# Kernel tuning notes

Hardware: AMD Instinct MI355X
Metric: run time of the kernel (lower is better)

Reference implementation:

```python
import jax, jax.numpy as jnp
import numpy as np

N = 100000
E = 3200000
F_IN, H1, H2, C = 128, 64, 32, 10


def setup_inputs() -> dict:
    key = jax.random.key(0)
    ks = jax.random.split(key, 8)
    x = jax.random.normal(ks[0], (N, F_IN), dtype=jnp.float32)
    edge_index = jax.random.randint(ks[1], (2, E), 0, N, dtype=jnp.int64)
    W1 = jax.random.normal(ks[2], (F_IN, H1), dtype=jnp.float32) / np.sqrt(F_IN)
    b1 = jnp.zeros((H1,), dtype=jnp.float32)
    W2 = jax.random.normal(ks[3], (H1, H2), dtype=jnp.float32) / np.sqrt(H1)
    b2 = jnp.zeros((H2,), dtype=jnp.float32)
    Wc = jax.random.normal(ks[4], (H2, C), dtype=jnp.float32) / np.sqrt(H2)
    bc = jnp.zeros((C,), dtype=jnp.float32)
    return {"x": x, "edge_index": edge_index, "W1": W1, "b1": b1,
            "W2": W2, "b2": b2, "Wc": Wc, "bc": bc}


def gcn_conv(x, src, dst, W, b, n):
    # PyG GCNConv: x' = D^{-1/2} (A + I) D^{-1/2} (X W) + b
    h = x @ W                                        # [N, H]
    ones = jnp.ones((src.shape[0],), dtype=h.dtype)
    deg = jax.ops.segment_sum(ones, dst, num_segments=n) + 1.0  # +1 self loop
    dinv = jax.lax.rsqrt(deg)                        # deg >= 1, safe
    norm = dinv[src] * dinv[dst]                     # [E]
    msg = h[src] * norm[:, None]                     # [E, H] gather + scale
    agg = jax.ops.segment_sum(msg, dst, num_segments=n)
    # self-loop contribution: norm_ii = 1/deg_i
    out = agg + h * (dinv * dinv)[:, None]
    return out + b


def reference(x, edge_index, W1, b1, W2, b2, Wc, bc):
    n = x.shape[0]
    src, dst = edge_index[0], edge_index[1]
    h = gcn_conv(x, src, dst, W1, b1, n)
    h = jax.nn.relu(h)
    # dropout is identity in eval mode (training=False)
    h = gcn_conv(h, src, dst, W2, b2, n)
    h = jax.nn.relu(h)
    logits = h @ Wc + bc
    return jax.nn.log_softmax(logits, axis=1)
```

## Files before the change

kernel.cpp:

```cpp
#include <hip/hip_runtime.h>


#define BSHIFT 8
#define BMASK 255
#define NBUCK_MAX 512
#define TILE 4096
#define EPT 16
#define NPW 4
#define SCAP 12288

__device__ __forceinline__ unsigned pack_bf16(float lo, float hi) {
    unsigned ul = __float_as_uint(lo);
    ul = (ul + 0x7FFFu + ((ul >> 16) & 1u)) >> 16;
    unsigned uh = __float_as_uint(hi);
    uh = ((uh + 0x7FFFu + ((uh >> 16) & 1u)) >> 16) << 16;
    return ul | uh;
}

__global__ void k_hist(const int* __restrict__ dst, int* __restrict__ bcnt, int E) {
    __shared__ int h[NBUCK_MAX];
    for (int i = threadIdx.x; i < NBUCK_MAX; i += blockDim.x) h[i] = 0;
    __syncthreads();
    for (int e = blockIdx.x * blockDim.x + threadIdx.x; e < E; e += gridDim.x * blockDim.x)
        atomicAdd(&h[dst[e] >> BSHIFT], 1);
    __syncthreads();
    for (int i = threadIdx.x; i < NBUCK_MAX; i += blockDim.x)
        if (h[i]) atomicAdd(&bcnt[i], h[i]);
}

__global__ __launch_bounds__(256) void k_binA(const int* __restrict__ src,
                                              const int* __restrict__ dst,
                                              const int* __restrict__ bcnt,
                                              int* __restrict__ gcur0,
                                              int* __restrict__ binned, int E) {
    __shared__ int hist[NBUCK_MAX];
    __shared__ int lbase[NBUCK_MAX];
    __shared__ int gbase[NBUCK_MAX];
    __shared__ int gdelta[NBUCK_MAX];
    __shared__ int cnt2[NBUCK_MAX];
    __shared__ int scanb[256];
    __shared__ int scanc[256];
    __shared__ int stage[TILE];
    __shared__ unsigned short sbucket[TILE];

    int t = threadIdx.x;
    for (int i = t; i < NBUCK_MAX; i += 256) { hist[i] = 0; cnt2[i] = 0; }
    int c0 = bcnt[2 * t], c1 = bcnt[2 * t + 1];
    int cs = c0 + c1;
    scanc[t] = cs;
    __syncthreads();
    for (int o = 1; o < 256; o <<= 1) {
        int u = (t >= o) ? scanc[t - o] : 0;
        __syncthreads();
        scanc[t] += u;
        __syncthreads();
    }
    int ex2 = scanc[t] - cs;
    gbase[2 * t] = ex2;
    gbase[2 * t + 1] = ex2 + c0;
    __syncthreads();

    int tileStart = blockIdx.x * TILE;
    int cntTile = min(TILE, E - tileStart);

    int vals[EPT];
    int bks[EPT];
#pragma unroll
    for (int i = 0; i < EPT; i++) {
        int e = tileStart + t + i * 256;
        if (e < E) {
            int s = src[e], d = dst[e];
            vals[i] = s | ((d & BMASK) << 17);
            bks[i] = d >> BSHIFT;
            atomicAdd(&hist[bks[i]], 1);
        } else bks[i] = -1;
    }
    __syncthreads();

    int a0 = hist[2 * t], a1 = hist[2 * t + 1];
    int ts = a0 + a1;
    scanb[t] = ts;
    __syncthreads();
    for (int o = 1; o < 256; o <<= 1) {
        int u = (t >= o) ? scanb[t - o] : 0;
        __syncthreads();
        scanb[t] += u;
        __syncthreads();
    }
    int ex = scanb[t] - ts;
    lbase[2 * t] = ex;
    lbase[2 * t + 1] = ex + a0;
    __syncthreads();

    for (int b = t; b < NBUCK_MAX; b += 256) {
        int c = hist[b];
        int g = c ? (gbase[b] + atomicAdd(&gcur0[b], c)) : 0;
        gdelta[b] = g - lbase[b];
    }
#pragma unroll
    for (int i = 0; i < EPT; i++) {
        if (bks[i] >= 0) {
            int rr = atomicAdd(&cnt2[bks[i]], 1);
            int slot = lbase[bks[i]] + rr;
            stage[slot] = vals[i];
            sbucket[slot] = (unsigned short)bks[i];
        }
    }
    __syncthreads();
    for (int i = t; i < cntTile; i += 256) {
        int b = sbucket[i];
        binned[gdelta[b] + i] = stage[i];
    }
}

__global__ __launch_bounds__(256) void k_sortcsr(const int* __restrict__ bcnt,
                                                 const int* __restrict__ binned,
                                                 int* __restrict__ rowptr,
                                                 float* __restrict__ dinv,
                                                 int* __restrict__ csr, int n, int E) {
    __shared__ int cnt[256];
    __shared__ int sc[256];
    __shared__ int rpl[256];
    __shared__ int lcur[256];
    __shared__ int gbase[NBUCK_MAX];
    __shared__ int scanc[256];
    __shared__ int stage2[SCAP];
    int b = blockIdx.x, t = threadIdx.x;
    cnt[t] = 0; lcur[t] = 0;
    int c0 = bcnt[2 * t], c1 = bcnt[2 * t + 1];
    int cs = c0 + c1;
    scanc[t] = cs;
    __syncthreads();
    for (int o = 1; o < 256; o <<= 1) {
        int u = (t >= o) ? scanc[t - o] : 0;
        __syncthreads();
        scanc[t] += u;
        __syncthreads();
    }
    int ex2 = scanc[t] - cs;
    gbase[2 * t] = ex2;
    gbase[2 * t + 1] = ex2 + c0;
    __syncthreads();

    int beg = gbase[b];
    int end = (b + 1 < NBUCK_MAX) ? gbase[b + 1] : E;
    for (int i = beg + t; i < end; i += 256)
        atomicAdd(&cnt[(binned[i] >> 17) & BMASK], 1);
    __syncthreads();
    int v = cnt[t];
    sc[t] = v;
    __syncthreads();
    for (int o = 1; o < 256; o <<= 1) {
        int u = (t >= o) ? sc[t - o] : 0;
        __syncthreads();
        sc[t] += u;
        __syncthreads();
    }
    int rp = beg + sc[t] - v;
    rpl[t] = rp;
    int g = (b << BSHIFT) + t;
    if (g < n) {
        rowptr[g] = rp;
        dinv[g] = rsqrtf((float)v + 1.0f);
        if (g == n - 1) rowptr[n] = E;
    }
    __syncthreads();
    for (int i = beg + t; i < end; i += 256) {
        int vv = binned[i];
        int ln = (vv >> 17) & BMASK;
        int k = atomicAdd(&lcur[ln], 1);
        int idx = rpl[ln] + k - beg;
        if (idx < SCAP) stage2[idx] = vv & 0x1FFFF;
        else            csr[beg + idx] = vv & 0x1FFFF;
    }
    __syncthreads();
    int cc = end - beg;
    for (int i = t; i < cc; i += 256)
        if (i < SCAP) csr[beg + i] = stage2[i];
}

template<int K, int M, int R>
__global__ __launch_bounds__(256) void k_gemm(const float* __restrict__ X,
                                              const float* __restrict__ W,
                                              const float* __restrict__ dinv,
                                              unsigned* __restrict__ hsb, int n) {
    constexpr int MW = M / 4;
    __shared__ float Ws[K * M];
    for (int i = threadIdx.x; i < K * M; i += 256) Ws[i] = W[i];
    __syncthreads();
    int w = threadIdx.x >> 6, lane = threadIdx.x & 63;
    int wo = w * MW;
    int r0 = blockIdx.x * (64 * R) + lane;
    float acc[R][MW];
#pragma unroll
    for (int i = 0; i < R; i++)
#pragma unroll
        for (int j = 0; j < MW; j++) acc[i][j] = 0.f;

    for (int k = 0; k < K; k += 4) {
        float4 xv[R];
#pragma unroll
        for (int i = 0; i < R; i++) {
            int rr = r0 + 64 * i;
            xv[i] = (rr < n) ? *(const float4*)(X + (size_t)rr * K + k)
                             : make_float4(0.f, 0.f, 0.f, 0.f);
        }
#pragma unroll
        for (int kk = 0; kk < 4; kk++) {
#pragma unroll
            for (int j = 0; j < MW; j += 4) {
                float4 wv = *(const float4*)&Ws[(k + kk) * M + wo + j];
#pragma unroll
                for (int i = 0; i < R; i++) {
                    float xs = (kk == 0) ? xv[i].x : (kk == 1) ? xv[i].y
                             : (kk == 2) ? xv[i].z : xv[i].w;
                    acc[i][j + 0] += xs * wv.x;
                    acc[i][j + 1] += xs * wv.y;
                    acc[i][j + 2] += xs * wv.z;
                    acc[i][j + 3] += xs * wv.w;
                }
            }
        }
    }
#pragma unroll
    for (int i = 0; i < R; i++) {
        int rr = r0 + 64 * i;
        if (rr < n) {
            float di = dinv[rr];
            unsigned p[MW / 2];
#pragma unroll
            for (int jj = 0; jj < MW / 2; jj++)
                p[jj] = pack_bf16(acc[i][2 * jj] * di, acc[i][2 * jj + 1] * di);
            unsigned* hr = hsb + (size_t)rr * (M / 2) + wo / 2;
#pragma unroll
            for (int jj = 0; jj < MW / 2; jj += 4)
                *(uint4*)(hr + jj) = make_uint4(p[jj], p[jj + 1], p[jj + 2], p[jj + 3]);
        }
    }
}

#define ACC8(V) \
    acc[0] += __uint_as_float((V).x << 16);  acc[1] += __uint_as_float((V).x & 0xFFFF0000u); \
    acc[2] += __uint_as_float((V).y << 16);  acc[3] += __uint_as_float((V).y & 0xFFFF0000u); \
    acc[4] += __uint_as_float((V).z << 16);  acc[5] += __uint_as_float((V).z & 0xFFFF0000u); \
    acc[6] += __uint_as_float((V).w << 16);  acc[7] += __uint_as_float((V).w & 0xFFFF0000u);

__global__ __launch_bounds__(256) void k_agg64f(
        const int* __restrict__ rowptr, const int* __restrict__ csr,
        const uint4* __restrict__ hsb, const float* __restrict__ dinv,
        const float* __restrict__ b1, const float* __restrict__ W2,
        unsigned* __restrict__ hsb2, int n) {
    int wid = (blockIdx.x * blockDim.x + threadIdx.x) >> 6;
    int lane = threadIdx.x & 63;
    int q = lane >> 3, r = lane & 7;
    int d0 = wid * NPW;
    if (d0 >= n) return;
    float w2r[8][4];
    float b1r[8];
#pragma unroll
    for (int i = 0; i < 8; i++) {
        b1r[i] = b1[8 * r + i];
#pragma unroll
        for (int jj = 0; jj < 4; jj++)
            w2r[i][jj] = W2[(8 * r + i) * 32 + 4 * q + jj];
    }
    int dend = min(d0 + NPW, n);
    int rp = rowptr[min(d0 + min(lane, NPW), n)];
    int beg = __shfl(rp, 0, 64);
    int end = __shfl(rp, 1, 64);
    int cc = min(end - beg, 64);
    int idxv = (lane < cc) ? csr[beg + lane] : 0;
    for (int d = d0; d < dend; d++) {
        int kk = d - d0;
        int nbeg = __shfl(rp, min(kk + 1, NPW), 64);
        int nend = __shfl(rp, min(kk + 2, NPW), 64);
        int ncc = min(nend - nbeg, 64);
        int nidxv = 0;
        if (d + 1 < dend) nidxv = (lane < ncc) ? csr[nbeg + lane] : 0;
        uint4 wsf = hsb[(size_t)d * 8 + r];
        float di = dinv[d];
        float acc[8];
#pragma unroll
        for (int i = 0; i < 8; i++) acc[i] = 0.f;
        int j = 0;
        for (; j + 16 <= cc; j += 16) {
            int sA = __shfl(idxv, j + q, 64);
            int sB = __shfl(idxv, j + 8 + q, 64);
            uint4 wA = hsb[(size_t)sA * 8 + r];
            uint4 wB = hsb[(size_t)sB * 8 + r];
            ACC8(wA)
            ACC8(wB)
        }
        {
            int tA = j + q, tB = j + 8 + q;
            int sA = __shfl(idxv, tA & 63, 64);
            int sB = __shfl(idxv, tB & 63, 64);
            if (tA < cc) { uint4 wv = hsb[(size_t)sA * 8 + r]; ACC8(wv) }
            if (tB < cc) { uint4 wv = hsb[(size_t)sB * 8 + r]; ACC8(wv) }
        }
        for (int c = beg + 64; c < end; c += 16) {
            if (c + q < end)     { uint4 wv = hsb[(size_t)csr[c + q] * 8 + r]; ACC8(wv) }
            if (c + 8 + q < end) { uint4 wv = hsb[(size_t)csr[c + 8 + q] * 8 + r]; ACC8(wv) }
        }
#pragma unroll
        for (int i = 0; i < 8; i++) {
            acc[i] += __shfl_xor(acc[i], 8, 64);
            acc[i] += __shfl_xor(acc[i], 16, 64);
            acc[i] += __shfl_xor(acc[i], 32, 64);
        }
        ACC8(wsf)
        float v[8];
#pragma unroll
        for (int i = 0; i < 8; i++) v[i] = fmaxf(acc[i] * di + b1r[i], 0.f);
        float h[4] = {0.f, 0.f, 0.f, 0.f};
#pragma unroll
        for (int i = 0; i < 8; i++)
#pragma unroll
            for (int jj = 0; jj < 4; jj++) h[jj] += v[i] * w2r[i][jj];
#pragma unroll
        for (int jj = 0; jj < 4; jj++) {
            h[jj] += __shfl_xor(h[jj], 1, 64);
            h[jj] += __shfl_xor(h[jj], 2, 64);
            h[jj] += __shfl_xor(h[jj], 4, 64);
        }
        if (r == 0) {
            unsigned p0 = pack_bf16(h[0] * di, h[1] * di);
            unsigned p1 = pack_bf16(h[2] * di, h[3] * di);
            *(uint2*)(hsb2 + (size_t)d * 16 + 2 * q) = make_uint2(p0, p1);
        }
        beg = nbeg; end = nend; cc = ncc; idxv = nidxv;
    }
}

__global__ __launch_bounds__(256) void k_agg32f(
        const int* __restrict__ rowptr, const int* __restrict__ csr,
        const uint4* __restrict__ hsb2, const float* __restrict__ dinv,
        const float* __restrict__ b2, const float* __restrict__ Wc,
        const float* __restrict__ bc, float* __restrict__ out, int n) {
    int wid = (blockIdx.x * blockDim.x + threadIdx.x) >> 6;
    int lane = threadIdx.x & 63;
    int q = lane >> 2, r = lane & 3;
    int d0 = wid * NPW;
    if (d0 >= n) return;
    float wcr[8];
    float b2r[8];
    float bcr = (q < 10) ? bc[q] : 0.f;
#pragma unroll
    for (int i = 0; i < 8; i++) {
        b2r[i] = b2[8 * r + i];
        wcr[i] = (q < 10) ? Wc[(8 * r + i) * 10 + q] : 0.f;
    }
    int dend = min(d0 + NPW, n);
    int rp = rowptr[min(d0 + min(lane, NPW), n)];
    int beg = __shfl(rp, 0, 64);
    int end = __shfl(rp, 1, 64);
    int cc = min(end - beg, 64);
    int idxv = (lane < cc) ? csr[beg + lane] : 0;
    for (int d = d0; d < dend; d++) {
        int kk = d - d0;
        int nbeg = __shfl(rp, min(kk + 1, NPW), 64);
        int nend = __shfl(rp, min(kk + 2, NPW), 64);
        int ncc = min(nend - nbeg, 64);
        int nidxv = 0;
        if (d + 1 < dend) nidxv = (lane < ncc) ? csr[nbeg + lane] : 0;
        uint4 wsf = hsb2[(size_t)d * 4 + r];
        float di = dinv[d];
        float acc[8];
#pragma unroll
        for (int i = 0; i < 8; i++) acc[i] = 0.f;
        int j = 0;
        for (; j + 32 <= cc; j += 32) {
            int sA = __shfl(idxv, j + q, 64);
            int sB = __shfl(idxv, j + 16 + q, 64);
            uint4 wA = hsb2[(size_t)sA * 4 + r];
            uint4 wB = hsb2[(size_t)sB * 4 + r];
            ACC8(wA)
            ACC8(wB)
        }
        {
            int tA = j + q, tB = j + 16 + q;
            int sA = __shfl(idxv, tA & 63, 64);
            int sB = __shfl(idxv, tB & 63, 64);
            if (tA < cc) { uint4 wv = hsb2[(size_t)sA * 4 + r]; ACC8(wv) }
            if (tB < cc) { uint4 wv = hsb2[(size_t)sB * 4 + r]; ACC8(wv) }
        }
        for (int c = beg + 64; c < end; c += 32) {
            if (c + q < end)      { uint4 wv = hsb2[(size_t)csr[c + q] * 4 + r]; ACC8(wv) }
            if (c + 16 + q < end) { uint4 wv = hsb2[(size_t)csr[c + 16 + q] * 4 + r]; ACC8(wv) }
        }
#pragma unroll
        for (int i = 0; i < 8; i++) {
            acc[i] += __shfl_xor(acc[i], 4, 64);
            acc[i] += __shfl_xor(acc[i], 8, 64);
            acc[i] += __shfl_xor(acc[i], 16, 64);
            acc[i] += __shfl_xor(acc[i], 32, 64);
        }
        ACC8(wsf)
        float part = 0.f;
#pragma unroll
        for (int i = 0; i < 8; i++) {
            float v = fmaxf(acc[i] * di + b2r[i], 0.f);
            part += v * wcr[i];
        }
        part += __shfl_xor(part, 1, 64);
        part += __shfl_xor(part, 2, 64);
        float mylogit = part + bcr;
        float m = -1e30f;
        float l[10];
#pragma unroll
        for (int c = 0; c < 10; c++) {
            l[c] = __shfl(mylogit, 4 * c, 64);
            m = fmaxf(m, l[c]);
        }
        float ssum = 0.f;
#pragma unroll
        for (int c = 0; c < 10; c++) ssum += __expf(l[c] - m);
        float lse = m + __logf(ssum);
        if (r == 0 && q < 10) out[(size_t)d * 10 + q] = mylogit - lse;
        beg = nbeg; end = nend; cc = ncc; idxv = nidxv;
    }
}

extern "C" void kernel_launch(void* const* d_in, const int* in_sizes, int n_in,
                              void* d_out, int out_size, void* d_ws, size_t ws_size,
                              hipStream_t stream) {
    const float* x  = (const float*)d_in[0];
    const int*   ei = (const int*)d_in[1];
    const float* W1 = (const float*)d_in[2];
    const float* b1 = (const float*)d_in[3];
    const float* W2 = (const float*)d_in[4];
    const float* b2 = (const float*)d_in[5];
    const float* Wc = (const float*)d_in[6];
    const float* bc = (const float*)d_in[7];
    float* out = (float*)d_out;

    const int N = in_sizes[0] / 128;
    const int E = in_sizes[1] / 2;
    const int* src = ei;
    const int* dst = ei + E;

    const int NBUCK = (N + BMASK) >> BSHIFT;
    const int NTILE = (E + TILE - 1) / TILE;
    const int NW = (N + NPW - 1) / NPW;

    char* ws = (char*)d_ws;
    size_t off = 0;
    auto alloc = [&](size_t elems) {
        void* p = ws + off;
        off += ((elems * 4 + 1023) & ~(size_t)1023);
        return p;
    };
    float*    dinv   = (float*)alloc(N);
    int*      bcnt   = (int*)alloc(NBUCK_MAX);
    int*      gcur0  = (int*)alloc(NBUCK_MAX);
    int*      rowptr = (int*)alloc(N + 1);
    int*      binned = (int*)alloc(E);
    int*      csr    = (int*)alloc(E);
    unsigned* hsb    = (unsigned*)alloc((size_t)N * 32);
    unsigned* hsb2   = (unsigned*)alloc((size_t)N * 16);

    hipMemsetAsync(bcnt, 0, sizeof(int) * NBUCK_MAX * 2, stream);

    k_hist<<<512, 256, 0, stream>>>(dst, bcnt, E);
    k_binA<<<NTILE, 256, 0, stream>>>(src, dst, bcnt, gcur0, binned, E);
    k_sortcsr<<<NBUCK, 256, 0, stream>>>(bcnt, binned, rowptr, dinv, csr, N, E);

    k_gemm<128, 64, 2><<<(N + 127) / 128, 256, 0, stream>>>(x, W1, dinv, hsb, N);
    k_agg64f<<<(NW * 64 + 255) / 256, 256, 0, stream>>>(rowptr, csr, (const uint4*)hsb,
                                                        dinv, b1, W2, hsb2, N);
    k_agg32f<<<(NW * 64 + 255) / 256, 256, 0, stream>>>(rowptr, csr, (const uint4*)hsb2,
                                                        dinv, b2, Wc, bc, out, N);
}
```

Baseline: 359.6 us.

## Split layer-1 aggregation into feature-sliced gather passes plus separate finalize kernel

```diff
diff --git a/kernel.cpp b/kernel.cpp
--- a/kernel.cpp
+++ b/kernel.cpp
@@ -183,7 +183,7 @@
 __global__ __launch_bounds__(256) void k_gemm(const float* __restrict__ X,
                                               const float* __restrict__ W,
                                               const float* __restrict__ dinv,
-                                              unsigned* __restrict__ hsb, int n) {
+                                              unsigned* __restrict__ hsbS, int n) {
     constexpr int MW = M / 4;
     __shared__ float Ws[K * M];
     for (int i = threadIdx.x; i < K * M; i += 256) Ws[i] = W[i];
@@ -231,23 +231,71 @@
 #pragma unroll
             for (int jj = 0; jj < MW / 2; jj++)
                 p[jj] = pack_bf16(acc[i][2 * jj] * di, acc[i][2 * jj + 1] * di);
-            unsigned* hr = hsb + (size_t)rr * (M / 2) + wo / 2;
-#pragma unroll
-            for (int jj = 0; jj < MW / 2; jj += 4)
-                *(uint4*)(hr + jj) = make_uint4(p[jj], p[jj + 1], p[jj + 2], p[jj + 3]);
-        }
-    }
-}
-
-#define ACC8(V) \
-    acc[0] += __uint_as_float((V).x << 16);  acc[1] += __uint_as_float((V).x & 0xFFFF0000u); \
-    acc[2] += __uint_as_float((V).y << 16);  acc[3] += __uint_as_float((V).y & 0xFFFF0000u); \
-    acc[4] += __uint_as_float((V).z << 16);  acc[5] += __uint_as_float((V).z & 0xFFFF0000u); \
-    acc[6] += __uint_as_float((V).w << 16);  acc[7] += __uint_as_float((V).w & 0xFFFF0000u);
-
-__global__ __launch_bounds__(256) void k_agg64f(
+            unsigned* hr = hsbS + ((size_t)w * n + rr) * 8;
+            *(uint4*)(hr + 0) = make_uint4(p[0], p[1], p[2], p[3]);
+            *(uint4*)(hr + 4) = make_uint4(p[4], p[5], p[6], p[7]);
+        }
+    }
+}
+
+__global__ __launch_bounds__(256) void k_aggp(
         const int* __restrict__ rowptr, const int* __restrict__ csr,
-        const uint4* __restrict__ hsb, const float* __restrict__ dinv,
+        const unsigned* __restrict__ hsbS, float* __restrict__ agg, int n) {
+    int b = blockIdx.x;
+    int s = b & 3;
+    int ib = b >> 2;
+    int wid = ib * 4 + (threadIdx.x >> 6);
+    int lane = threadIdx.x & 63;
+    int e = lane >> 3, f = lane & 7;
+    int d0 = wid * NPW;
+    if (d0 >= n) return;
+    const unsigned* tab = hsbS + (size_t)s * n * 8;
+    int dend = min(d0 + NPW, n);
+    int rp = rowptr[min(d0 + min(lane, NPW), n)];
+    int beg = __shfl(rp, 0, 64);
+    int end = __shfl(rp, 1, 64);
+    int cc = min(end - beg, 64);
+    int idxv = (lane < cc) ? __builtin_nontemporal_load(&csr[beg + lane]) : 0;
+    for (int d = d0; d < dend; d++) {
+        int kk = d - d0;
+        int nbeg = __shfl(rp, min(kk + 1, NPW), 64);
+        int nend = __shfl(rp, min(kk + 2, NPW), 64);
+        int ncc = min(nend - nbeg, 64);
+        int nidxv = 0;
+        if (d + 1 < dend) nidxv = (lane < ncc) ? __builtin_nontemporal_load(&csr[nbeg + lane]) : 0;
+        unsigned wsf = tab[(size_t)d * 8 + f];
+        float a0 = 0.f, a1 = 0.f;
+#pragma unroll
+        for (int g = 0; g < 8; g++) {
+            int slot = 8 * g + e;
+            int sg = __shfl(idxv, slot, 64);
+            if (slot < cc) {
+                unsigned wv = tab[(size_t)sg * 8 + f];
+                a0 += __uint_as_float(wv << 16);
+                a1 += __uint_as_float(wv & 0xFFFF0000u);
+            }
+        }
+        for (int c = beg + 64; c < end; c += 8) {
+            if (c + e < end) {
+                int sx = __builtin_nontemporal_load(&csr[c + e]);
+                unsigned wv = tab[(size_t)sx * 8 + f];
+                a0 += __uint_as_float(wv << 16);
+                a1 += __uint_as_float(wv & 0xFFFF0000u);
+            }
+        }
+        a0 += __shfl_xor(a0, 8, 64);  a1 += __shfl_xor(a1, 8, 64);
+        a0 += __shfl_xor(a0, 16, 64); a1 += __shfl_xor(a1, 16, 64);
+        a0 += __shfl_xor(a0, 32, 64); a1 += __shfl_xor(a1, 32, 64);
+        a0 += __uint_as_float(wsf << 16);
+        a1 += __uint_as_float(wsf & 0xFFFF0000u);
+        if (e == 0)
+            *(float2*)(agg + ((size_t)d * 4 + s) * 16 + 2 * f) = make_float2(a0, a1);
+        beg = nbeg; end = nend; cc = ncc; idxv = nidxv;
+    }
+}
+
+__global__ __launch_bounds__(256) void k_fin64(
+        const float* __restrict__ agg, const float* __restrict__ dinv,
         const float* __restrict__ b1, const float* __restrict__ W2,
         unsigned* __restrict__ hsb2, int n) {
     int wid = (blockIdx.x * blockDim.x + threadIdx.x) >> 6;
@@ -265,53 +313,19 @@
             w2r[i][jj] = W2[(8 * r + i) * 32 + 4 * q + jj];
     }
     int dend = min(d0 + NPW, n);
-    int rp = rowptr[min(d0 + min(lane, NPW), n)];
-    int beg = __shfl(rp, 0, 64);
-    int end = __shfl(rp, 1, 64);
-    int cc = min(end - beg, 64);
-    int idxv = (lane < cc) ? csr[beg + lane] : 0;
     for (int d = d0; d < dend; d++) {
-        int kk = d - d0;
-        int nbeg = __shfl(rp, min(kk + 1, NPW), 64);
-        int nend = __shfl(rp, min(kk + 2, NPW), 64);
-        int ncc = min(nend - nbeg, 64);
-        int nidxv = 0;
-        if (d + 1 < dend) nidxv = (lane < ncc) ? csr[nbeg + lane] : 0;
-        uint4 wsf = hsb[(size_t)d * 8 + r];
+        float4 x0 = *(const float4*)(agg + (size_t)d * 64 + 8 * r);
+        float4 x1 = *(const float4*)(agg + (size_t)d * 64 + 8 * r + 4);
         float di = dinv[d];
-        float acc[8];
-#pragma unroll
-        for (int i = 0; i < 8; i++) acc[i] = 0.f;
-        int j = 0;
-        for (; j + 16 <= cc; j += 16) {
-            int sA = __shfl(idxv, j + q, 64);
-            int sB = __shfl(idxv, j + 8 + q, 64);
-            uint4 wA = hsb[(size_t)sA * 8 + r];
-            uint4 wB = hsb[(size_t)sB * 8 + r];
-            ACC8(wA)
-            ACC8(wB)
-        }
-        {
-            int tA = j + q, tB = j + 8 + q;
-            int sA = __shfl(idxv, tA & 63, 64);
-            int sB = __shfl(idxv, tB & 63, 64);
-            if (tA < cc) { uint4 wv = hsb[(size_t)sA * 8 + r]; ACC8(wv) }
-            if (tB < cc) { uint4 wv = hsb[(size_t)sB * 8 + r]; ACC8(wv) }
-        }
-        for (int c = beg + 64; c < end; c += 16) {
-            if (c + q < end)     { uint4 wv = hsb[(size_t)csr[c + q] * 8 + r]; ACC8(wv) }
-            if (c + 8 + q < end) { uint4 wv = hsb[(size_t)csr[c + 8 + q] * 8 + r]; ACC8(wv) }
-        }
-#pragma unroll
-        for (int i = 0; i < 8; i++) {
-            acc[i] += __shfl_xor(acc[i], 8, 64);
-            acc[i] += __shfl_xor(acc[i], 16, 64);
-            acc[i] += __shfl_xor(acc[i], 32, 64);
-        }
-        ACC8(wsf)
         float v[8];
-#pragma unroll
-        for (int i = 0; i < 8; i++) v[i] = fmaxf(acc[i] * di + b1r[i], 0.f);
+        v[0] = fmaxf(x0.x * di + b1r[0], 0.f);
+        v[1] = fmaxf(x0.y * di + b1r[1], 0.f);
+        v[2] = fmaxf(x0.z * di + b1r[2], 0.f);
+        v[3] = fmaxf(x0.w * di + b1r[3], 0.f);
+        v[4] = fmaxf(x1.x * di + b1r[4], 0.f);
+        v[5] = fmaxf(x1.y * di + b1r[5], 0.f);
+        v[6] = fmaxf(x1.z * di + b1r[6], 0.f);
+        v[7] = fmaxf(x1.w * di + b1r[7], 0.f);
         float h[4] = {0.f, 0.f, 0.f, 0.f};
 #pragma unroll
         for (int i = 0; i < 8; i++)
@@ -328,9 +342,14 @@
             unsigned p1 = pack_bf16(h[2] * di, h[3] * di);
             *(uint2*)(hsb2 + (size_t)d * 16 + 2 * q) = make_uint2(p0, p1);
         }
-        beg = nbeg; end = nend; cc = ncc; idxv = nidxv;
-    }
-}
+    }
+}
+
+#define ACC8(V) \
+    acc[0] += __uint_as_float((V).x << 16);  acc[1] += __uint_as_float((V).x & 0xFFFF0000u); \
+    acc[2] += __uint_as_float((V).y << 16);  acc[3] += __uint_as_float((V).y & 0xFFFF0000u); \
+    acc[4] += __uint_as_float((V).z << 16);  acc[5] += __uint_as_float((V).z & 0xFFFF0000u); \
+    acc[6] += __uint_as_float((V).w << 16);  acc[7] += __uint_as_float((V).w & 0xFFFF0000u);
 
 __global__ __launch_bounds__(256) void k_agg32f(
         const int* __restrict__ rowptr, const int* __restrict__ csr,
@@ -442,6 +461,7 @@
     const int NBUCK = (N + BMASK) >> BSHIFT;
     const int NTILE = (E + TILE - 1) / TILE;
     const int NW = (N + NPW - 1) / NPW;
+    const int NBS = (N + 15) / 16;
 
     char* ws = (char*)d_ws;
     size_t off = 0;
@@ -456,8 +476,9 @@
     int*      rowptr = (int*)alloc(N + 1);
     int*      binned = (int*)alloc(E);
     int*      csr    = (int*)alloc(E);
-    unsigned* hsb    = (unsigned*)alloc((size_t)N * 32);
+    unsigned* hsbS   = (unsigned*)alloc((size_t)N * 32);
     unsigned* hsb2   = (unsigned*)alloc((size_t)N * 16);
+    float*    agg    = (float*)alloc((size_t)N * 64);
 
     hipMemsetAsync(bcnt, 0, sizeof(int) * NBUCK_MAX * 2, stream);
 
@@ -465,9 +486,9 @@
     k_binA<<<NTILE, 256, 0, stream>>>(src, dst, bcnt, gcur0, binned, E);
     k_sortcsr<<<NBUCK, 256, 0, stream>>>(bcnt, binned, rowptr, dinv, csr, N, E);
 
-    k_gemm<128, 64, 2><<<(N + 127) / 128, 256, 0, stream>>>(x, W1, dinv, hsb, N);
-    k_agg64f<<<(NW * 64 + 255) / 256, 256, 0, stream>>>(rowptr, csr, (const uint4*)hsb,
-                                                        dinv, b1, W2, hsb2, N);
+    k_gemm<128, 64, 2><<<(N + 127) / 128, 256, 0, stream>>>(x, W1, dinv, hsbS, N);
+    k_aggp<<<4 * NBS, 256, 0, stream>>>(rowptr, csr, hsbS, agg, N);
+    k_fin64<<<(NW * 64 + 255) / 256, 256, 0, stream>>>(agg, dinv, b1, W2, hsb2, N);
     k_agg32f<<<(NW * 64 + 255) / 256, 256, 0, stream>>>(rowptr, csr, (const uint4*)hsb2,
                                                         dinv, b2, Wc, bc, out, N);
 }
```

Result: slower. 449.3 us (+25.0%).
